# Performance work log

Measured on AMD Instinct MI355X. Metric: run time of the kernel, lower is better.

The kernel has to match this reference:

```python
import jax, jax.numpy as jnp
import numpy as np

# --- dims (match init_kwargs) ---
B_, L_, IN_DIM = 32, 2048, 6
D_MODEL, N_LAYERS, D_STATE, D_CONV, EXPAND = 256, 4, 16, 4, 2
D_INNER = D_MODEL * EXPAND  # 512
SENT, TA, FH = 768, 12, 256
C1, C2, OUT = 128, 64, 3
LN_EPS = 1e-5


def layernorm(x, g, b):
    m = x.mean(-1, keepdims=True)
    v = ((x - m) ** 2).mean(-1, keepdims=True)
    return (x - m) * jax.lax.rsqrt(v + LN_EPS) * g + b


def ssm_layer(x, Wi, cw, cb, Wx, Wdt, bdt, A_log, Dp, Wo, g, b):
    """SimpleSSMBlock forward. x: (B, L, d_model)."""
    Bn, L, _ = x.shape
    xz = x @ Wi.T                               # (B, L, 2*d_inner)
    xp, z = jnp.split(xz, 2, axis=-1)
    # causal depthwise conv1d (left pad d_conv-1, truncate to L)
    xc = jnp.transpose(xp, (0, 2, 1))           # (B, d_inner, L)
    xc = jax.lax.conv_general_dilated(
        xc, cw, (1,), [(D_CONV - 1, 0)],
        dimension_numbers=('NCH', 'OIH', 'NCH'),
        feature_group_count=D_INNER) + cb[None, :, None]
    xc = jax.nn.silu(jnp.transpose(xc, (0, 2, 1)))  # (B, L, d_inner)
    A = -jnp.exp(A_log)                          # (d_inner, d_state)
    dt = jax.nn.softplus(xc @ Wdt.T + bdt)       # (B, L, d_inner)
    bx = xc @ Wx.T                               # (B, L, 2*d_state)
    Bm, Cm = jnp.split(bx, 2, axis=-1)

    def step(h, inp):
        dt_t, B_t, C_t, x_t = inp                # (B,d_inner),(B,d_state),(B,d_state),(B,d_inner)
        dA = jnp.exp(A[None] * dt_t[..., None])  # (B, d_inner, d_state)
        h = dA * h + (dt_t[..., None] * B_t[:, None, :]) * x_t[..., None]
        y_t = jnp.einsum('bdn,bn->bd', h, C_t)
        return h, y_t

    h0 = jnp.zeros((Bn, D_INNER, D_STATE), x.dtype)
    _, ys = jax.lax.scan(step, h0, (dt.transpose(1, 0, 2), Bm.transpose(1, 0, 2),
                                    Cm.transpose(1, 0, 2), xc.transpose(1, 0, 2)))
    y = ys.transpose(1, 0, 2) + xc * Dp          # (B, L, d_inner)
    y = y * jax.nn.silu(z)
    return layernorm(y @ Wo.T + x, g, b)


def setup_inputs() -> dict:
    key = jax.random.key(0)
    ks = iter(jax.random.split(key, 64))
    def rn(shape, scale=0.02):
        return (jax.random.normal(next(ks), shape, jnp.float32) * scale)
    dt_bias = jnp.exp(jax.random.uniform(next(ks), (N_LAYERS, D_INNER))
                      * (np.log(0.1) - np.log(0.001)) + np.log(0.001)).astype(jnp.float32)
    A_log = jnp.tile(jnp.log(jnp.arange(1, D_STATE + 1, dtype=jnp.float32))[None, None, :],
                     (N_LAYERS, D_INNER, 1))
    return {
        'x': jax.random.normal(next(ks), (B_, L_, IN_DIM), jnp.float32),
        'sentiment': jax.random.normal(next(ks), (B_, SENT), jnp.float32),
        'ta_features': jax.random.normal(next(ks), (B_, TA), jnp.float32),
        'input_proj_w': rn((D_MODEL, IN_DIM), 0.1), 'input_proj_b': jnp.zeros(D_MODEL),
        'in_proj_w': rn((N_LAYERS, 2 * D_INNER, D_MODEL)),
        'conv_w': rn((N_LAYERS, D_INNER, 1, D_CONV), 0.1),
        'conv_b': jnp.zeros((N_LAYERS, D_INNER)),
        'x_proj_w': rn((N_LAYERS, 2 * D_STATE, D_INNER)),
        'dt_proj_w': rn((N_LAYERS, D_INNER, D_INNER), D_INNER ** -0.5),
        'dt_proj_b': dt_bias,
        'A_log': A_log,
        'D': jnp.ones((N_LAYERS, D_INNER)),
        'out_proj_w': rn((N_LAYERS, D_MODEL, D_INNER)),
        'ln_g': jnp.ones((N_LAYERS, D_MODEL)), 'ln_b': jnp.zeros((N_LAYERS, D_MODEL)),
        'enc_norm_g': jnp.ones(D_MODEL), 'enc_norm_b': jnp.zeros(D_MODEL),
        'fus_w1': rn((FH, D_MODEL + SENT + TA)), 'fus_b1': jnp.zeros(FH),
        'fus_ln_g': jnp.ones(FH), 'fus_ln_b': jnp.zeros(FH),
        'fus_w2': rn((FH, FH)), 'fus_b2': jnp.zeros(FH),
        'cls_w1': rn((C1, FH)), 'cls_b1': jnp.zeros(C1),
        'cls_w2': rn((C2, C1)), 'cls_b2': jnp.zeros(C2),
        'cls_w3': rn((OUT, C2)), 'cls_b3': jnp.zeros(OUT),
    }


def reference(x, sentiment, ta_features, input_proj_w, input_proj_b, in_proj_w,
              conv_w, conv_b, x_proj_w, dt_proj_w, dt_proj_b, A_log, D, out_proj_w,
              ln_g, ln_b, enc_norm_g, enc_norm_b, fus_w1, fus_b1, fus_ln_g, fus_ln_b,
              fus_w2, fus_b2, cls_w1, cls_b1, cls_w2, cls_b2, cls_w3, cls_b3):
    # MambaEncoder (dropout = identity in eval)
    h = x @ input_proj_w.T + input_proj_b       # (B, L, d_model)
    for i in range(N_LAYERS):
        h = ssm_layer(h, in_proj_w[i], conv_w[i], conv_b[i], x_proj_w[i],
                      dt_proj_w[i], dt_proj_b[i], A_log[i], D[i], out_proj_w[i],
                      ln_g[i], ln_b[i])
    tick = layernorm(h[:, -1], enc_norm_g, enc_norm_b)  # final state
    # FusionLayer (concat_project)
    comb = jnp.concatenate([tick, sentiment, ta_features], axis=-1)
    f = jax.nn.gelu(comb @ fus_w1.T + fus_b1, approximate=False)
    f = layernorm(f, fus_ln_g, fus_ln_b)
    f = f @ fus_w2.T + fus_b2
    # classifier
    c = jax.nn.gelu(f @ cls_w1.T + cls_b1, approximate=False)
    c = jax.nn.gelu(c @ cls_w2.T + cls_b2, approximate=False)
    return c @ cls_w3.T + cls_b3                 # (B, 3)
```

## Files before the change

### kernel.cpp

```cpp
#include <hip/hip_runtime.h>
#include <hip/hip_bf16.h>
#include <math.h>

#define B_SZ   32
#define L_SEQ  2048
#define BL     (B_SZ * L_SEQ)
#define D_MODEL 256
#define D_INNER 512
#define D_STATE 16
#define D_CONV  4
#define LN_EPS  1e-5f
#define SEG    64
#define TSEG   (L_SEQ / SEG)

typedef short  s16x8 __attribute__((ext_vector_type(8)));
typedef float  f32x4 __attribute__((ext_vector_type(4)));

__device__ __forceinline__ unsigned short f2bf(float x) {
    unsigned int u = __float_as_uint(x);
    unsigned int r = (u + 0x7fffu + ((u >> 16) & 1u)) >> 16;
    return (unsigned short)r;
}
__device__ __forceinline__ float bf2f(unsigned short h) {
    return __uint_as_float((unsigned int)h << 16);
}
__device__ __forceinline__ float4 bf2f4(ushort4 u) {
    return make_float4(bf2f(u.x), bf2f(u.y), bf2f(u.z), bf2f(u.w));
}

__device__ __forceinline__ void async_ld16(const unsigned short* g, unsigned short* l) {
    __builtin_amdgcn_global_load_lds(
        (const __attribute__((address_space(1))) unsigned int*)g,
        (__attribute__((address_space(3))) unsigned int*)l, 16, 0, 0);
}

__global__ __launch_bounds__(256) void convert_w_kernel(
    const float* __restrict__ src, unsigned short* __restrict__ hi, int n)
{
    int i = blockIdx.x * 256 + threadIdx.x;
    if (i < n) hi[i] = f2bf(src[i]);
}

__global__ __launch_bounds__(256) void input_proj_kernel(
    const float* __restrict__ x, const float* __restrict__ W,
    const float* __restrict__ b, float* __restrict__ h,
    unsigned short* __restrict__ hh)
{
    size_t row = blockIdx.x;
    int c = threadIdx.x;
    const float* xr = x + row * 6;
    const float* wr = W + c * 6;
    float acc = b[c];
#pragma unroll
    for (int k = 0; k < 6; k++) acc += xr[k] * wr[k];
    h[row * D_MODEL + c] = acc;
    hh[row * D_MODEL + c] = f2bf(acc);
}

#define GBUF (128 * 32)
template <int EPI>
__global__ __launch_bounds__(256) void gemm_bf16s(
    const unsigned short* __restrict__ Ahi, int lda,
    const unsigned short* __restrict__ Whi,
    const float* __restrict__ bias, const float* __restrict__ res,
    float* __restrict__ C, int ldc,
    unsigned short* __restrict__ U1, unsigned short* __restrict__ U2,
    int M, int N, int K)
{
    __shared__ unsigned short Ah[2 * GBUF];
    __shared__ unsigned short Bh[2 * GBUF];
    const int tid = threadIdx.x;
    const int m0 = blockIdx.y * 128, n0 = blockIdx.x * 128;
    const int lane = tid & 63, wave = tid >> 6;
    const int quad = lane >> 4, l15 = lane & 15;
    const int wm = wave & 1, wn = wave >> 1;

    const int r16 = lane >> 2;
    const int kg  = (lane & 3) ^ ((lane >> 3) & 3);
    const unsigned short* gsrc; unsigned short* lbase; int ld;
    if (wave == 0)      { gsrc = Ahi + (size_t)m0 * lda;        ld = lda; lbase = Ah; }
    else if (wave == 1) { gsrc = Ahi + (size_t)(m0 + 64) * lda; ld = lda; lbase = Ah + 64 * 32; }
    else if (wave == 2) { gsrc = Whi + (size_t)n0 * K;          ld = K;   lbase = Bh; }
    else                { gsrc = Whi + (size_t)(n0 + 64) * K;   ld = K;   lbase = Bh + 64 * 32; }
    const unsigned short* gp = gsrc + (size_t)r16 * ld + kg * 8;
    const size_t ld16 = (size_t)ld * 16;

    f32x4 acc[4][4];
#pragma unroll
    for (int mi = 0; mi < 4; mi++)
#pragma unroll
        for (int ni = 0; ni < 4; ni++) acc[mi][ni] = (f32x4){0.f, 0.f, 0.f, 0.f};

    const int sx = (l15 >> 1) & 3;
    const int nK = K >> 5;

#pragma unroll
    for (int j = 0; j < 4; j++)
        async_ld16(gp + (size_t)j * ld16, lbase + j * 512);

    for (int ki = 0; ki < nK; ki++) {
        const int p = ki & 1;
        __syncthreads();
        if (ki + 1 < nK) {
            const size_t ko = (size_t)(ki + 1) << 5;
#pragma unroll
            for (int j = 0; j < 4; j++)
                async_ld16(gp + (size_t)j * ld16 + ko, lbase + (1 - p) * GBUF + j * 512);
        }

        s16x8 ah[4], bh[4];
#pragma unroll
        for (int i = 0; i < 4; i++) {
            const int ra = p * GBUF + (wm * 64 + i * 16 + l15) * 32 + ((quad ^ sx) << 3);
            const int rb = p * GBUF + (wn * 64 + i * 16 + l15) * 32 + ((quad ^ sx) << 3);
            ah[i] = *(s16x8*)&Ah[ra];
            bh[i] = *(s16x8*)&Bh[rb];
        }
#pragma unroll
        for (int mi = 0; mi < 4; mi++)
#pragma unroll
            for (int ni = 0; ni < 4; ni++)
                acc[mi][ni] = __builtin_amdgcn_mfma_f32_16x16x32_bf16(
                    ah[mi], bh[ni], acc[mi][ni], 0, 0, 0);
    }

#pragma unroll
    for (int mi = 0; mi < 4; mi++) {
        const int mrow = m0 + wm * 64 + mi * 16 + quad * 4;
#pragma unroll
        for (int ni = 0; ni < 4; ni++) {
            const int ncol = n0 + wn * 64 + ni * 16 + l15;
#pragma unroll
            for (int r = 0; r < 4; r++) {
                float v = acc[mi][ni][r];
                if (EPI == 0) {
                    if (ncol < 512)
                        U1[(size_t)(mrow + r) * 512 + ncol] = f2bf(v);
                    else
                        U2[(size_t)(mrow + r) * 512 + (ncol - 512)] = f2bf(v);
                } else if (EPI == 1) {
                    v += bias[ncol];
                    v = (v > 20.f) ? v : log1pf(expf(v));
                    U1[(size_t)(mrow + r) * 512 + ncol] = f2bf(v);
                } else {
                    v += res[(size_t)(mrow + r) * ldc + ncol];
                    C[(size_t)(mrow + r) * ldc + ncol] = v;
                }
            }
        }
    }
}

#define XBUFA (64 * 32)
#define XBUFB (32 * 32)
__global__ __launch_bounds__(256) void xproj_mfma_kernel(
    const unsigned short* __restrict__ Ahi,
    const unsigned short* __restrict__ Whi,
    float* __restrict__ bc)
{
    __shared__ unsigned short Ah[2 * XBUFA];
    __shared__ unsigned short Bh[2 * XBUFB];
    const int tid = threadIdx.x;
    const int m0 = blockIdx.x * 64;
    const int lane = tid & 63, wave = tid >> 6;
    const int quad = lane >> 4, l15 = lane & 15;

    const int r16 = lane >> 2;
    const int kg  = (lane & 3) ^ ((lane >> 3) & 3);
    const unsigned short* gsrc = nullptr; unsigned short* lbase = nullptr; int bufsz = 0;
    if (wave == 0)      { gsrc = Ahi + (size_t)m0 * 512;        lbase = Ah;           bufsz = XBUFA; }
    else if (wave == 1) { gsrc = Ahi + (size_t)(m0 + 32) * 512; lbase = Ah + 32 * 32; bufsz = XBUFA; }
    else if (wave == 2) { gsrc = Whi;                           lbase = Bh;           bufsz = XBUFB; }
    const unsigned short* gp = gsrc ? gsrc + (size_t)r16 * 512 + kg * 8 : nullptr;

    f32x4 acc[2];
    acc[0] = (f32x4){0.f, 0.f, 0.f, 0.f};
    acc[1] = (f32x4){0.f, 0.f, 0.f, 0.f};
    const int sx = (l15 >> 1) & 3;

    if (wave < 3) {
#pragma unroll
        for (int j = 0; j < 2; j++)
            async_ld16(gp + (size_t)j * (16 * 512), lbase + j * 512);
    }

    for (int ki = 0; ki < 16; ki++) {
        const int p = ki & 1;
        __syncthreads();
        if (ki + 1 < 16 && wave < 3) {
            const size_t ko = (size_t)(ki + 1) << 5;
#pragma unroll
            for (int j = 0; j < 2; j++)
                async_ld16(gp + (size_t)j * (16 * 512) + ko,
                           lbase + (1 - p) * bufsz + j * 512);
        }

        const int ra = p * XBUFA + (wave * 16 + l15) * 32 + ((quad ^ sx) << 3);
        s16x8 ah = *(s16x8*)&Ah[ra];
#pragma unroll
        for (int ni = 0; ni < 2; ni++) {
            const int rb = p * XBUFB + (ni * 16 + l15) * 32 + ((quad ^ sx) << 3);
            s16x8 bh = *(s16x8*)&Bh[rb];
            acc[ni] = __builtin_amdgcn_mfma_f32_16x16x32_bf16(ah, bh, acc[ni], 0, 0, 0);
        }
    }

#pragma unroll
    for (int ni = 0; ni < 2; ni++) {
        const int ncol = ni * 16 + l15;
#pragma unroll
        for (int r = 0; r < 4; r++) {
            const int mrow = m0 + wave * 16 + quad * 4 + r;
            bc[(size_t)mrow * 32 + ncol] = acc[ni][r];
        }
    }
}

__global__ __launch_bounds__(256) void conv_silu_kernel(
    const unsigned short* __restrict__ xp, const float* __restrict__ cw,
    const float* __restrict__ cb,
    unsigned short* __restrict__ xch)
{
    size_t idx = (size_t)blockIdx.x * 256 + threadIdx.x;
    const int d4 = (int)(idx & 127) << 2;
    const int row = (int)(idx >> 7);
    const int t = row & (L_SEQ - 1);

    const float4 wA = *(const float4*)(cw + (d4 + 0) * 4);
    const float4 wB = *(const float4*)(cw + (d4 + 1) * 4);
    const float4 wC = *(const float4*)(cw + (d4 + 2) * 4);
    const float4 wD = *(const float4*)(cw + (d4 + 3) * 4);
    const float4 bias4 = *(const float4*)(cb + d4);
    const float4 zero = make_float4(0.f, 0.f, 0.f, 0.f);

    const unsigned short* p = xp + (size_t)row * 512 + d4;
    float4 x3 = bf2f4(*(const ushort4*)p);
    float4 x2 = (t >= 1) ? bf2f4(*(const ushort4*)(p - 512))  : zero;
    float4 x1 = (t >= 2) ? bf2f4(*(const ushort4*)(p - 1024)) : zero;
    float4 x0 = (t >= 3) ? bf2f4(*(const ushort4*)(p - 1536)) : zero;

    float4 a;
    a.x = bias4.x + x0.x * wA.x + x1.x * wA.y + x2.x * wA.z + x3.x * wA.w;
    a.y = bias4.y + x0.y * wB.x + x1.y * wB.y + x2.y * wB.z + x3.y * wB.w;
    a.z = bias4.z + x0.z * wC.x + x1.z * wC.y + x2.z * wC.z + x3.z * wC.w;
    a.w = bias4.w + x0.w * wD.x + x1.w * wD.y + x2.w * wD.z + x3.w * wD.w;

    float4 o;
    o.x = a.x / (1.f + __expf(-a.x));
    o.y = a.y / (1.f + __expf(-a.y));
    o.z = a.z / (1.f + __expf(-a.z));
    o.w = a.w / (1.f + __expf(-a.w));

    ushort4 h4;
    h4.x = f2bf(o.x); h4.y = f2bf(o.y); h4.z = f2bf(o.z); h4.w = f2bf(o.w);
    *(ushort4*)(xch + (size_t)row * 512 + d4) = h4;
}

__global__ __launch_bounds__(256) void scan_pass1_kernel(
    const unsigned short* __restrict__ dtb,
    const unsigned short* __restrict__ xch,
    const float* __restrict__ bc,
    unsigned short* __restrict__ Pbuf,
    unsigned short* __restrict__ Qbuf,
    int nb)
{
    const int tid = threadIdx.x;
    const int dp = tid >> 1, nh = tid & 1;
    const int s = blockIdx.x & (SEG - 1);
    const int g = (blockIdx.x >> 6) & 1;
    const int b = blockIdx.x >> 7;
    const int d0 = g * 256 + dp * 2;

    const size_t row0 = (size_t)b * L_SEQ + (size_t)s * TSEG;
    const unsigned short* dtp = dtb + row0 * 512 + d0;
    const unsigned short* xhp = xch + row0 * 512 + d0;
    const float* bp = bc + row0 * 32 + nh * 8;

    float h0[8], h1[8];
#pragma unroll
    for (int j = 0; j < 8; j++) { h0[j] = 0.f; h1[j] = 0.f; }
    float Pe0 = 1.f, Pe1 = 1.f;

#pragma unroll 2
    for (int t = 0; t < TSEG; t++) {
        const ushort2 dt2 = *(const ushort2*)(dtp + (size_t)t * 512);
        const ushort2 xc2 = *(const ushort2*)(xhp + (size_t)t * 512);
        const float4 B0 = *(const float4*)(bp + (size_t)t * 32);
        const float4 B1 = *(const float4*)(bp + (size_t)t * 32 + 4);
        {
            const float dt = bf2f(dt2.x), xcv = bf2f(xc2.x);
            const float E = __expf(-dt);
            Pe0 *= E;
            const float E2 = E * E, E4 = E2 * E2;
            const float E3 = E2 * E, E5 = E4 * E, E6 = E4 * E2, E7 = E4 * E3, E8 = E4 * E4;
            const float base = nh ? E8 : 1.f;
            const float dtxc = dt * xcv;
            h0[0] = fmaf(base * E,  h0[0], dtxc * B0.x);
            h0[1] = fmaf(base * E2, h0[1], dtxc * B0.y);
            h0[2] = fmaf(base * E3, h0[2], dtxc * B0.z);
            h0[3] = fmaf(base * E4, h0[3], dtxc * B0.w);
            h0[4] = fmaf(base * E5, h0[4], dtxc * B1.x);
            h0[5] = fmaf(base * E6, h0[5], dtxc * B1.y);
            h0[6] = fmaf(base * E7, h0[6], dtxc * B1.z);
            h0[7] = fmaf(base * E8, h0[7], dtxc * B1.w);
        }
        {
            const float dt = bf2f(dt2.y), xcv = bf2f(xc2.y);
            const float E = __expf(-dt);
            Pe1 *= E;
            const float E2 = E * E, E4 = E2 * E2;
            const float E3 = E2 * E, E5 = E4 * E, E6 = E4 * E2, E7 = E4 * E3, E8 = E4 * E4;
            const float base = nh ? E8 : 1.f;
            const float dtxc = dt * xcv;
            h1[0] = fmaf(base * E,  h1[0], dtxc * B0.x);
            h1[1] = fmaf(base * E2, h1[1], dtxc * B0.y);
            h1[2] = fmaf(base * E3, h1[2], dtxc * B0.z);
            h1[3] = fmaf(base * E4, h1[3], dtxc * B0.w);
            h1[4] = fmaf(base * E5, h1[4], dtxc * B1.x);
            h1[5] = fmaf(base * E6, h1[5], dtxc * B1.y);
            h1[6] = fmaf(base * E7, h1[6], dtxc * B1.z);
            h1[7] = fmaf(base * E8, h1[7], dtxc * B1.w);
        }
    }

    const int N = nb * 512 * 16;
    const size_t base_s = (size_t)s * N;
    {
        const float P2 = Pe0 * Pe0, P4 = P2 * P2;
        const float P3 = P2 * Pe0, P5 = P4 * Pe0, P6 = P4 * P2, P7 = P4 * P3, P8 = P4 * P4;
        const float pb = nh ? P8 : 1.f;
        const int idx = (b * 512 + d0) * 16 + nh * 8;
        ushort4 pa, pbv, qa, qb;
        pa.x = f2bf(pb * Pe0); pa.y = f2bf(pb * P2); pa.z = f2bf(pb * P3); pa.w = f2bf(pb * P4);
        pbv.x = f2bf(pb * P5); pbv.y = f2bf(pb * P6); pbv.z = f2bf(pb * P7); pbv.w = f2bf(pb * P8);
        qa.x = f2bf(h0[0]); qa.y = f2bf(h0[1]); qa.z = f2bf(h0[2]); qa.w = f2bf(h0[3]);
        qb.x = f2bf(h0[4]); qb.y = f2bf(h0[5]); qb.z = f2bf(h0[6]); qb.w = f2bf(h0[7]);
        *(ushort4*)(Pbuf + base_s + idx)     = pa;
        *(ushort4*)(Pbuf + base_s + idx + 4) = pbv;
        *(ushort4*)(Qbuf + base_s + idx)     = qa;
        *(ushort4*)(Qbuf + base_s + idx + 4) = qb;
    }
    {
        const float P2 = Pe1 * Pe1, P4 = P2 * P2;
        const float P3 = P2 * Pe1, P5 = P4 * Pe1, P6 = P4 * P2, P7 = P4 * P3, P8 = P4 * P4;
        const float pb = nh ? P8 : 1.f;
        const int idx = (b * 512 + d0 + 1) * 16 + nh * 8;
        ushort4 pa, pbv, qa, qb;
        pa.x = f2bf(pb * Pe1); pa.y = f2bf(pb * P2); pa.z = f2bf(pb * P3); pa.w = f2bf(pb * P4);
        pbv.x = f2bf(pb * P5); pbv.y = f2bf(pb * P6); pbv.z = f2bf(pb * P7); pbv.w = f2bf(pb * P8);
        qa.x = f2bf(h1[0]); qa.y = f2bf(h1[1]); qa.z = f2bf(h1[2]); qa.w = f2bf(h1[3]);
        qb.x = f2bf(h1[4]); qb.y = f2bf(h1[5]); qb.z = f2bf(h1[6]); qb.w = f2bf(h1[7]);
        *(ushort4*)(Pbuf + base_s + idx)     = pa;
        *(ushort4*)(Pbuf + base_s + idx + 4) = pbv;
        *(ushort4*)(Qbuf + base_s + idx)     = qa;
        *(ushort4*)(Qbuf + base_s + idx + 4) = qb;
    }
}

__global__ __launch_bounds__(256) void scan_pass2_kernel(
    unsigned short* __restrict__ Pbuf, const unsigned short* __restrict__ Qbuf,
    int N)
{
    const int idx = blockIdx.x * 256 + threadIdx.x;
    float run = 0.f;
#pragma unroll 8
    for (int s = 0; s < SEG; s++) {
        const float p = bf2f(Pbuf[(size_t)s * N + idx]);
        const float q = bf2f(Qbuf[(size_t)s * N + idx]);
        Pbuf[(size_t)s * N + idx] = f2bf(run);
        run = fmaf(p, run, q);
    }
}

__global__ __launch_bounds__(256) void scan_pass3_kernel(
    const unsigned short* __restrict__ dtb,
    const unsigned short* __restrict__ zb,
    unsigned short* ych,
    const float* __restrict__ bc,
    const float* __restrict__ Dp,
    const unsigned short* __restrict__ Hin,
    int nb)
{
    const int tid = threadIdx.x;
    const int dp = tid >> 1, nh = tid & 1;
    const int s = blockIdx.x & (SEG - 1);
    const int g = (blockIdx.x >> 6) & 1;
    const int b = blockIdx.x >> 7;
    const int d0 = g * 256 + dp * 2;

    const float2 Dd2 = *(const float2*)(Dp + d0);
    const int N = nb * 512 * 16;
    const size_t base_s = (size_t)s * N;
    const int idx0 = (b * 512 + d0) * 16 + nh * 8;
    const int idx1 = idx0 + 16;
    ushort4 ha0 = *(const ushort4*)(Hin + base_s + idx0);
    ushort4 hb0 = *(const ushort4*)(Hin + base_s + idx0 + 4);
    ushort4 ha1 = *(const ushort4*)(Hin + base_s + idx1);
    ushort4 hb1 = *(const ushort4*)(Hin + base_s + idx1 + 4);
    float h0[8] = {bf2f(ha0.x), bf2f(ha0.y), bf2f(ha0.z), bf2f(ha0.w),
                   bf2f(hb0.x), bf2f(hb0.y), bf2f(hb0.z), bf2f(hb0.w)};
    float h1[8] = {bf2f(ha1.x), bf2f(ha1.y), bf2f(ha1.z), bf2f(ha1.w),
                   bf2f(hb1.x), bf2f(hb1.y), bf2f(hb1.z), bf2f(hb1.w)};

    const size_t row0 = (size_t)b * L_SEQ + (size_t)s * TSEG;
    const unsigned short* dtp = dtb + row0 * 512 + d0;
    const unsigned short* zp  = zb + row0 * 512 + d0;
    unsigned short* yhp = ych + row0 * 512 + d0;
    const float* bp = bc + row0 * 32 + nh * 8;
    const float* cp = bc + row0 * 32 + 16 + nh * 8;

#pragma unroll 2
    for (int t = 0; t < TSEG; t++) {
        const ushort2 dt2 = *(const ushort2*)(dtp + (size_t)t * 512);
        const ushort2 xc2 = *(const ushort2*)(yhp + (size_t)t * 512);
        const ushort2 z2  = *(const ushort2*)(zp + (size_t)t * 512);
        const float4 B0 = *(const float4*)(bp + (size_t)t * 32);
        const float4 B1 = *(const float4*)(bp + (size_t)t * 32 + 4);
        const float4 C0 = *(const float4*)(cp + (size_t)t * 32);
        const float4 C1 = *(const float4*)(cp + (size_t)t * 32 + 4);

        float pv0, pv1;
        {
            const float dt = bf2f(dt2.x), xcv = bf2f(xc2.x);
            const float E = __expf(-dt);
            const float E2 = E * E, E4 = E2 * E2;
            const float E3 = E2 * E, E5 = E4 * E, E6 = E4 * E2, E7 = E4 * E3, E8 = E4 * E4;
            const float base = nh ? E8 : 1.f;
            const float dtxc = dt * xcv;
            h0[0] = fmaf(base * E,  h0[0], dtxc * B0.x);
            h0[1] = fmaf(base * E2, h0[1], dtxc * B0.y);
            h0[2] = fmaf(base * E3, h0[2], dtxc * B0.z);
            h0[3] = fmaf(base * E4, h0[3], dtxc * B0.w);
            h0[4] = fmaf(base * E5, h0[4], dtxc * B1.x);
            h0[5] = fmaf(base * E6, h0[5], dtxc * B1.y);
            h0[6] = fmaf(base * E7, h0[6], dtxc * B1.z);
            h0[7] = fmaf(base * E8, h0[7], dtxc * B1.w);
            pv0 = h0[0] * C0.x + h0[1] * C0.y + h0[2] * C0.z + h0[3] * C0.w +
                  h0[4] * C1.x + h0[5] * C1.y + h0[6] * C1.z + h0[7] * C1.w;
        }
        {
            const float dt = bf2f(dt2.y), xcv = bf2f(xc2.y);
            const float E = __expf(-dt);
            const float E2 = E * E, E4 = E2 * E2;
            const float E3 = E2 * E, E5 = E4 * E, E6 = E4 * E2, E7 = E4 * E3, E8 = E4 * E4;
            const float base = nh ? E8 : 1.f;
            const float dtxc = dt * xcv;
            h1[0] = fmaf(base * E,  h1[0], dtxc * B0.x);
            h1[1] = fmaf(base * E2, h1[1], dtxc * B0.y);
            h1[2] = fmaf(base * E3, h1[2], dtxc * B0.z);
            h1[3] = fmaf(base * E4, h1[3], dtxc * B0.w);
            h1[4] = fmaf(base * E5, h1[4], dtxc * B1.x);
            h1[5] = fmaf(base * E6, h1[5], dtxc * B1.y);
            h1[6] = fmaf(base * E7, h1[6], dtxc * B1.z);
            h1[7] = fmaf(base * E8, h1[7], dtxc * B1.w);
            pv1 = h1[0] * C0.x + h1[1] * C0.y + h1[2] * C0.z + h1[3] * C0.w +
                  h1[4] * C1.x + h1[5] * C1.y + h1[6] * C1.z + h1[7] * C1.w;
        }
        pv0 += __shfl_xor(pv0, 1, 2);
        pv1 += __shfl_xor(pv1, 1, 2);
        if (nh == 0) {
            const float zv0 = bf2f(z2.x), zv1 = bf2f(z2.y);
            const float sig0 = 1.f / (1.f + __expf(-zv0));
            const float sig1 = 1.f / (1.f + __expf(-zv1));
            const float yv0 = (pv0 + bf2f(xc2.x) * Dd2.x) * (zv0 * sig0);
            const float yv1 = (pv1 + bf2f(xc2.y) * Dd2.y) * (zv1 * sig1);
            ushort2 yo;
            yo.x = f2bf(yv0); yo.y = f2bf(yv1);
            *(ushort2*)(yhp + (size_t)t * 512) = yo;
        }
    }
}

__global__ __launch_bounds__(256) void ln256_kernel(
    const float* __restrict__ in, const float* __restrict__ g,
    const float* __restrict__ b, float* __restrict__ out,
    unsigned short* __restrict__ hh)
{
    int wave = threadIdx.x >> 6, lane = threadIdx.x & 63;
    size_t row = (size_t)blockIdx.x * 4 + wave;
    const float* p = in + row * 256 + lane * 4;
    float4 v = *(const float4*)p;
    float s = v.x + v.y + v.z + v.w;
    float sq = v.x * v.x + v.y * v.y + v.z * v.z + v.w * v.w;
#pragma unroll
    for (int o = 32; o; o >>= 1) {
        s += __shfl_xor(s, o, 64);
        sq += __shfl_xor(sq, o, 64);
    }
    float m = s * (1.f / 256.f);
    float var = sq * (1.f / 256.f) - m * m;
    float rs = 1.f / sqrtf(var + LN_EPS);
    float4 gg = *(const float4*)(g + lane * 4);
    float4 bb = *(const float4*)(b + lane * 4);
    float4 o4;
    o4.x = (v.x - m) * rs * gg.x + bb.x;
    o4.y = (v.y - m) * rs * gg.y + bb.y;
    o4.z = (v.z - m) * rs * gg.z + bb.z;
    o4.w = (v.w - m) * rs * gg.w + bb.w;
    *(float4*)(out + row * 256 + lane * 4) = o4;
    ushort4 h4;
    h4.x = f2bf(o4.x); h4.y = f2bf(o4.y); h4.z = f2bf(o4.z); h4.w = f2bf(o4.w);
    *(ushort4*)(hh + row * 256 + lane * 4) = h4;
}

__device__ __forceinline__ float gelu_exact(float x) {
    return 0.5f * x * (1.f + erff(x * 0.70710678118654752f));
}

__global__ __launch_bounds__(256) void head_f1_kernel(
    const float* __restrict__ h, const float* __restrict__ sent,
    const float* __restrict__ ta,
    const float* __restrict__ eng, const float* __restrict__ enb,
    const float* __restrict__ w1, const float* __restrict__ b1,
    float* __restrict__ f1g)
{
    __shared__ __align__(16) float comb[1040];
    __shared__ float part[4][64];
    __shared__ float rs_[4], rq_[4];
    const int g = blockIdx.x, r = blockIdx.y, tid = threadIdx.x;

    float v = h[((size_t)r * L_SEQ + (L_SEQ - 1)) * 256 + tid];
    float s = v, sq = v * v;
#pragma unroll
    for (int o = 32; o; o >>= 1) { s += __shfl_xor(s, o, 64); sq += __shfl_xor(sq, o, 64); }
    if ((tid & 63) == 0) { rs_[tid >> 6] = s; rq_[tid >> 6] = sq; }
    __syncthreads();
    s = rs_[0] + rs_[1] + rs_[2] + rs_[3];
    sq = rq_[0] + rq_[1] + rq_[2] + rq_[3];
    float m = s * (1.f / 256.f);
    float var = sq * (1.f / 256.f) - m * m;
    float rstd = 1.f / sqrtf(var + LN_EPS);
    comb[tid] = (v - m) * rstd * eng[tid] + enb[tid];
    comb[256 + tid] = sent[(size_t)r * 768 + tid];
    comb[512 + tid] = sent[(size_t)r * 768 + 256 + tid];
    comb[768 + tid] = sent[(size_t)r * 768 + 512 + tid];
    if (tid < 12) comb[1024 + tid] = ta[(size_t)r * 12 + tid];
    __syncthreads();

    const int w = tid >> 6, cidx = tid & 63;
    const int col = g * 64 + cidx;
    const int k0 = w * 260;
    const int kn = (w < 3) ? 260 : 256;
    const float* wr = w1 + (size_t)col * 1036 + k0;
    const float* cc = comb + k0;
    float acc = 0.f;
    for (int k = 0; k < kn; k += 4) {
        float4 wv = *(const float4*)(wr + k);
        float4 cv = *(const float4*)(cc + k);
        acc += wv.x * cv.x + wv.y * cv.y + wv.z * cv.z + wv.w * cv.w;
    }
    part[w][cidx] = acc;
    __syncthreads();
    if (tid < 64) {
        float a = b1[g * 64 + tid] + part[0][tid] + part[1][tid] + part[2][tid] + part[3][tid];
        f1g[(size_t)r * 256 + g * 64 + tid] = gelu_exact(a);
    }
}

__global__ __launch_bounds__(256) void head_rest_kernel(
    const float* __restrict__ f1g,
    const float* __restrict__ lng, const float* __restrict__ lnb,
    const float* __restrict__ w2, const float* __restrict__ b2,
    const float* __restrict__ cw1, const float* __restrict__ cb1,
    const float* __restrict__ cw2, const float* __restrict__ cb2,
    const float* __restrict__ cw3, const float* __restrict__ cb3,
    float* __restrict__ out)
{
    __shared__ __align__(16) float comb[256];
    __shared__ __align__(16) float fbuf[256];
    __shared__ float rs_[4], rq_[4];
    const int r = blockIdx.x, tid = threadIdx.x;

    float f1 = f1g[(size_t)r * 256 + tid];
    float s = f1, sq = f1 * f1;
#pragma unroll
    for (int o = 32; o; o >>= 1) { s += __shfl_xor(s, o, 64); sq += __shfl_xor(sq, o, 64); }
    if ((tid & 63) == 0) { rs_[tid >> 6] = s; rq_[tid >> 6] = sq; }
    __syncthreads();
    s = rs_[0] + rs_[1] + rs_[2] + rs_[3];
    sq = rq_[0] + rq_[1] + rq_[2] + rq_[3];
    float m = s * (1.f / 256.f);
    float var = sq * (1.f / 256.f) - m * m;
    float rstd = 1.f / sqrtf(var + LN_EPS);
    fbuf[tid] = (f1 - m) * rstd * lng[tid] + lnb[tid];
    __syncthreads();

    float acc = b2[tid];
    {
        const float* wr = w2 + (size_t)tid * 256;
        for (int k = 0; k < 256; k += 4) {
            float4 wv = *(const float4*)(wr + k);
            float4 cv = *(const float4*)(fbuf + k);
            acc += wv.x * cv.x + wv.y * cv.y + wv.z * cv.z + wv.w * cv.w;
        }
    }
    __syncthreads();
    comb[tid] = acc;
    __syncthreads();

    if (tid < 128) {
        float a = cb1[tid];
        const float* wr = cw1 + (size_t)tid * 256;
        for (int k = 0; k < 256; k += 4) {
            float4 wv = *(const float4*)(wr + k);
            float4 cv = *(const float4*)(comb + k);
            a += wv.x * cv.x + wv.y * cv.y + wv.z * cv.z + wv.w * cv.w;
        }
        fbuf[tid] = gelu_exact(a);
    }
    __syncthreads();

    float c2v = 0.f;
    if (tid < 64) {
        float a = cb2[tid];
        const float* wr = cw2 + (size_t)tid * 128;
        for (int k = 0; k < 128; k += 4) {
            float4 wv = *(const float4*)(wr + k);
            float4 cv = *(const float4*)(fbuf + k);
            a += wv.x * cv.x + wv.y * cv.y + wv.z * cv.z + wv.w * cv.w;
        }
        c2v = gelu_exact(a);
    }
    __syncthreads();
    if (tid < 64) comb[tid] = c2v;
    __syncthreads();

    if (tid < 3) {
        float a = cb3[tid];
        const float* wr = cw3 + (size_t)tid * 64;
        for (int k = 0; k < 64; k++) a += wr[k] * comb[k];
        out[(size_t)r * 3 + tid] = a;
    }
}

extern "C" void kernel_launch(void* const* d_in, const int* in_sizes, int n_in,
                              void* d_out, int out_size, void* d_ws, size_t ws_size,
                              hipStream_t stream) {
    const float* x    = (const float*)d_in[0];
    const float* sent = (const float*)d_in[1];
    const float* ta   = (const float*)d_in[2];
    const float* ipw  = (const float*)d_in[3];
    const float* ipb  = (const float*)d_in[4];
    const float* inw  = (const float*)d_in[5];
    const float* cw   = (const float*)d_in[6];
    const float* cb   = (const float*)d_in[7];
    const float* xpw  = (const float*)d_in[8];
    const float* dtw  = (const float*)d_in[9];
    const float* dtb  = (const float*)d_in[10];
    const float* alog = (const float*)d_in[11];
    const float* Dp   = (const float*)d_in[12];
    const float* opw  = (const float*)d_in[13];
    const float* lng  = (const float*)d_in[14];
    const float* lnb  = (const float*)d_in[15];
    const float* eng  = (const float*)d_in[16];
    const float* enb  = (const float*)d_in[17];
    const float* fw1  = (const float*)d_in[18];
    const float* fb1  = (const float*)d_in[19];
    const float* flg  = (const float*)d_in[20];
    const float* flb  = (const float*)d_in[21];
    const float* fw2  = (const float*)d_in[22];
    const float* fb2  = (const float*)d_in[23];
    const float* cw1  = (const float*)d_in[24];
    const float* cb1  = (const float*)d_in[25];
    const float* cw2  = (const float*)d_in[26];
    const float* cb2  = (const float*)d_in[27];
    const float* cw3  = (const float*)d_in[28];
    const float* cb3  = (const float*)d_in[29];
    float* out = (float*)d_out;
    (void)alog;

    unsigned short* wbf = (unsigned short*)d_ws;
    const size_t OFF_IN = 0;
    const size_t OFF_DT = 1048576;
    const size_t OFF_OP = 2097152;
    const size_t OFF_XP = 2621440;
    const size_t WBF_TOTAL = 2686976;
    float* fbase = (float*)(wbf + WBF_TOTAL);

    int c = 1;
    while (c < 32 &&
           (WBF_TOTAL / 2 + (size_t)BL * 384 + ((size_t)BL / c) * 800 +
            (size_t)(B_SZ / c) * 524288 + 8192) * sizeof(float) > ws_size)
        c <<= 1;
    const size_t R = BL / c;
    const int nb = B_SZ / c;
    const int Nseg = nb * 512 * 16;

    float* hbuf  = fbase;
    unsigned short* hhbuf = (unsigned short*)(hbuf + (size_t)BL * 256);
    unsigned short* xpb = hhbuf + (size_t)BL * 256;
    unsigned short* zbb = xpb + R * 512;
    unsigned short* xcb = zbb + R * 512;
    float* bcbuf = (float*)(xcb + R * 512);
    unsigned short* Pbuf = (unsigned short*)(bcbuf + R * 32);
    unsigned short* Qbuf = Pbuf + (size_t)SEG * Nseg;
    float* f1g   = (float*)(Qbuf + (size_t)SEG * Nseg);
    unsigned short* dtbp = xpb;

    convert_w_kernel<<<4096, 256, 0, stream>>>(inw, wbf + OFF_IN, 1048576);
    convert_w_kernel<<<4096, 256, 0, stream>>>(dtw, wbf + OFF_DT, 1048576);
    convert_w_kernel<<<2048, 256, 0, stream>>>(opw, wbf + OFF_OP, 524288);
    convert_w_kernel<<<256, 256, 0, stream>>>(xpw, wbf + OFF_XP, 65536);

    input_proj_kernel<<<BL, 256, 0, stream>>>(x, ipw, ipb, hbuf, hhbuf);

    for (int l = 0; l < 4; l++) {
        const float* cw_l  = cw  + (size_t)l * 512 * 4;
        const float* cb_l  = cb  + (size_t)l * 512;
        const float* dtb_l = dtb + (size_t)l * 512;
        const float* Dp_l  = Dp  + (size_t)l * 512;
        const float* lng_l = lng + (size_t)l * 256;
        const float* lnb_l = lnb + (size_t)l * 256;
        const unsigned short* wih = wbf + OFF_IN + (size_t)l * 262144;
        const unsigned short* wdh = wbf + OFF_DT + (size_t)l * 262144;
        const unsigned short* woh = wbf + OFF_OP + (size_t)l * 131072;
        const unsigned short* wxh = wbf + OFF_XP + (size_t)l * 16384;

        for (int k = 0; k < c; k++) {
            float* hck = hbuf + (size_t)k * R * 256;
            unsigned short* hhk = hhbuf + (size_t)k * R * 256;

            gemm_bf16s<0><<<dim3(8, R / 128), 256, 0, stream>>>(
                hhk, 256, wih, nullptr, nullptr, nullptr, 0,
                xpb, zbb, (int)R, 1024, 256);
            conv_silu_kernel<<<(unsigned)(R / 2), 256, 0, stream>>>(
                xpb, cw_l, cb_l, xcb);
            gemm_bf16s<1><<<dim3(4, R / 128), 256, 0, stream>>>(
                xcb, 512, wdh, dtb_l, nullptr, nullptr, 0,
                dtbp, nullptr, (int)R, 512, 512);
            xproj_mfma_kernel<<<(unsigned)(R / 64), 256, 0, stream>>>(
                xcb, wxh, bcbuf);
            scan_pass1_kernel<<<(unsigned)(nb * 2 * SEG), 256, 0, stream>>>(
                dtbp, xcb, bcbuf, Pbuf, Qbuf, nb);
            scan_pass2_kernel<<<(unsigned)(Nseg / 256), 256, 0, stream>>>(
                Pbuf, Qbuf, Nseg);
            scan_pass3_kernel<<<(unsigned)(nb * 2 * SEG), 256, 0, stream>>>(
                dtbp, zbb, xcb, bcbuf, Dp_l, Pbuf, nb);
            gemm_bf16s<2><<<dim3(2, R / 128), 256, 0, stream>>>(
                xcb, 512, woh, nullptr, hck, hck, 256,
                nullptr, nullptr, (int)R, 256, 512);
            ln256_kernel<<<(unsigned)(R / 4), 256, 0, stream>>>(
                hck, lng_l, lnb_l, hck, hhk);
        }
    }

    head_f1_kernel<<<dim3(4, 32), 256, 0, stream>>>(
        hbuf, sent, ta, eng, enb, fw1, fb1, f1g);
    head_rest_kernel<<<32, 256, 0, stream>>>(
        f1g, flg, flb, fw2, fb2, cw1, cb1, cw2, cb2, cw3, cb3, out);
}
```

Baseline: 2.712 ms.

## Deepen GEMM async pipeline to four stages and vectorize epilogue stores

The bf16 GEMM kernel moves from a double-buffered LDS ring to a four-slot ring that prefetches three K-tiles ahead. Each iteration waits with explicit vmcnt counts instead of a full __syncthreads, so global-load latency can hide behind more MFMA work. The MFMA operands are also swapped so each lane holds four consecutive output columns, which lets the epilogue use 8- and 16-byte vector stores and loads instead of scalar ones. The cost is twice the LDS per block, which may lower occupancy. The hand-counted vmcnt waits also rely on async_ld16 issuing exactly one vm op each.

```diff
diff --git a/kernel.cpp b/kernel.cpp
--- a/kernel.cpp
+++ b/kernel.cpp
@@ -67,8 +67,8 @@
     unsigned short* __restrict__ U1, unsigned short* __restrict__ U2,
     int M, int N, int K)
 {
-    __shared__ unsigned short Ah[2 * GBUF];
-    __shared__ unsigned short Bh[2 * GBUF];
+    __shared__ unsigned short Ah[4 * GBUF];
+    __shared__ unsigned short Bh[4 * GBUF];
     const int tid = threadIdx.x;
     const int m0 = blockIdx.y * 128, n0 = blockIdx.x * 128;
     const int lane = tid & 63, wave = tid >> 6;
@@ -95,17 +95,26 @@
     const int nK = K >> 5;
 
 #pragma unroll
-    for (int j = 0; j < 4; j++)
-        async_ld16(gp + (size_t)j * ld16, lbase + j * 512);
+    for (int s = 0; s < 3; s++)
+#pragma unroll
+        for (int j = 0; j < 4; j++)
+            async_ld16(gp + (size_t)j * ld16 + ((size_t)s << 5),
+                       lbase + s * GBUF + j * 512);
 
     for (int ki = 0; ki < nK; ki++) {
-        const int p = ki & 1;
-        __syncthreads();
-        if (ki + 1 < nK) {
-            const size_t ko = (size_t)(ki + 1) << 5;
+        const int p = ki & 3;
+        const int rem = nK - 1 - ki;
+        if (rem >= 2)      asm volatile("s_waitcnt vmcnt(8)" ::: "memory");
+        else if (rem == 1) asm volatile("s_waitcnt vmcnt(4)" ::: "memory");
+        else               asm volatile("s_waitcnt vmcnt(0)" ::: "memory");
+        __builtin_amdgcn_s_barrier();
+
+        if (ki + 3 < nK) {
+            const size_t ko = (size_t)(ki + 3) << 5;
+            const int pn = (ki + 3) & 3;
 #pragma unroll
             for (int j = 0; j < 4; j++)
-                async_ld16(gp + (size_t)j * ld16 + ko, lbase + (1 - p) * GBUF + j * 512);
+                async_ld16(gp + (size_t)j * ld16 + ko, lbase + pn * GBUF + j * 512);
         }
 
         s16x8 ah[4], bh[4];
@@ -121,31 +130,40 @@
 #pragma unroll
             for (int ni = 0; ni < 4; ni++)
                 acc[mi][ni] = __builtin_amdgcn_mfma_f32_16x16x32_bf16(
-                    ah[mi], bh[ni], acc[mi][ni], 0, 0, 0);
+                    bh[ni], ah[mi], acc[mi][ni], 0, 0, 0);
     }
 
 #pragma unroll
     for (int mi = 0; mi < 4; mi++) {
-        const int mrow = m0 + wm * 64 + mi * 16 + quad * 4;
+        const int mrow = m0 + wm * 64 + mi * 16 + l15;
 #pragma unroll
         for (int ni = 0; ni < 4; ni++) {
-            const int ncol = n0 + wn * 64 + ni * 16 + l15;
-#pragma unroll
-            for (int r = 0; r < 4; r++) {
-                float v = acc[mi][ni][r];
-                if (EPI == 0) {
-                    if (ncol < 512)
-                        U1[(size_t)(mrow + r) * 512 + ncol] = f2bf(v);
-                    else
-                        U2[(size_t)(mrow + r) * 512 + (ncol - 512)] = f2bf(v);
-                } else if (EPI == 1) {
-                    v += bias[ncol];
-                    v = (v > 20.f) ? v : log1pf(expf(v));
-                    U1[(size_t)(mrow + r) * 512 + ncol] = f2bf(v);
-                } else {
-                    v += res[(size_t)(mrow + r) * ldc + ncol];
-                    C[(size_t)(mrow + r) * ldc + ncol] = v;
-                }
+            const int nc0 = n0 + wn * 64 + ni * 16 + quad * 4;
+            const f32x4 a = acc[mi][ni];
+            if (EPI == 0) {
+                ushort4 o;
+                o.x = f2bf(a[0]); o.y = f2bf(a[1]); o.z = f2bf(a[2]); o.w = f2bf(a[3]);
+                if (nc0 < 512)
+                    *(ushort4*)&U1[(size_t)mrow * 512 + nc0] = o;
+                else
+                    *(ushort4*)&U2[(size_t)mrow * 512 + (nc0 - 512)] = o;
+            } else if (EPI == 1) {
+                const float4 bi = *(const float4*)(bias + nc0);
+                float v0 = a[0] + bi.x, v1 = a[1] + bi.y;
+                float v2 = a[2] + bi.z, v3 = a[3] + bi.w;
+                v0 = (v0 > 20.f) ? v0 : log1pf(expf(v0));
+                v1 = (v1 > 20.f) ? v1 : log1pf(expf(v1));
+                v2 = (v2 > 20.f) ? v2 : log1pf(expf(v2));
+                v3 = (v3 > 20.f) ? v3 : log1pf(expf(v3));
+                ushort4 o;
+                o.x = f2bf(v0); o.y = f2bf(v1); o.z = f2bf(v2); o.w = f2bf(v3);
+                *(ushort4*)&U1[(size_t)mrow * 512 + nc0] = o;
+            } else {
+                const float4 rv = *(const float4*)(res + (size_t)mrow * ldc + nc0);
+                float4 cv;
+                cv.x = a[0] + rv.x; cv.y = a[1] + rv.y;
+                cv.z = a[2] + rv.z; cv.w = a[3] + rv.w;
+                *(float4*)(C + (size_t)mrow * ldc + nc0) = cv;
             }
         }
     }
```

After: 2.740 ms. No clear change (+1.0%).
